# Kernel tuning notes

Measured on AMD Instinct MI355X. Metric: run time of the kernel, lower is better.

## Reference

```python
import jax, jax.numpy as jnp
import numpy as np

B, T, I, H, O = 128, 512, 64, 1024, 12

def setup_inputs() -> dict:
    key = jax.random.key(0)
    ks = jax.random.split(key, 7)
    s_ih = 1.0 / np.sqrt(H)
    return {
        "x": jax.random.normal(ks[0], (B, T, I), dtype=jnp.float32),
        "W_ih": jax.random.normal(ks[1], (H, I), dtype=jnp.float32) * s_ih,
        "W_hh": jax.random.normal(ks[2], (H, H), dtype=jnp.float32) * s_ih,
        "b_ih": jax.random.normal(ks[3], (H,), dtype=jnp.float32) * s_ih,
        "b_hh": jax.random.normal(ks[4], (H,), dtype=jnp.float32) * s_ih,
        "W_out": jax.random.normal(ks[5], (O, H), dtype=jnp.float32) * s_ih,
        "b_out": jax.random.normal(ks[6], (O,), dtype=jnp.float32) * s_ih,
    }

def reference(x, W_ih, W_hh, b_ih, b_hh, W_out, b_out):
    # x: [B, T, I] (batch_first). Vanilla tanh RNN, h0 = 0.
    Bn, Tn, _ = x.shape
    Hn = W_hh.shape[0]
    # Precompute input projections for all timesteps (batched GEMM).
    xp = jnp.einsum('bti,hi->tbh', x, W_ih) + b_ih + b_hh  # [T, B, H]
    h0 = jnp.zeros((Bn, Hn), dtype=x.dtype)

    def step(h, xt):
        h_new = jnp.tanh(xt + h @ W_hh.T)
        return h_new, h_new

    _, hs = jax.lax.scan(step, h0, xp)  # hs: [T, B, H]
    hs = jnp.swapaxes(hs, 0, 1)         # [B, T, H]
    out = jnp.einsum('bth,oh->bto', hs, W_out) + b_out  # [B, T, O]
    return out.reshape(-1, 12)
```

## Files before the change

kernel.cpp:

```cpp
#include <hip/hip_runtime.h>
#include <hip/hip_bf16.h>

#define B_ 128
#define T_ 512
#define I_ 64
#define H_ 1024
#define O_ 12
#define XSTEP (I_ * B_)
#define RSLOT 16384
#define TIMEOUT 2000
#define OSTRIDE 193

typedef __attribute__((ext_vector_type(8))) short bf16x8;
typedef __attribute__((ext_vector_type(4))) float f32x4;

#define MFMA16 __builtin_amdgcn_mfma_f32_16x16x32_bf16

__device__ __forceinline__ float bf2f(unsigned short s) {
  unsigned u = ((unsigned)s) << 16; float f; __builtin_memcpy(&f, &u, 4); return f;
}
__device__ __forceinline__ unsigned short f2bf(float f) {
  unsigned u; __builtin_memcpy(&u, &f, 4);
  u += 0x7fffu + ((u >> 16) & 1u);
  return (unsigned short)(u >> 16);
}

__device__ __forceinline__ unsigned ldA32(const unsigned* p) {
  return __hip_atomic_load(p, __ATOMIC_RELAXED, __HIP_MEMORY_SCOPE_AGENT);
}
__device__ __forceinline__ void stA32(unsigned* p, unsigned v) {
  __hip_atomic_store(p, v, __ATOMIC_RELAXED, __HIP_MEMORY_SCOPE_AGENT);
}
__device__ __forceinline__ unsigned long long ldA64(const unsigned long long* p) {
  return __hip_atomic_load(p, __ATOMIC_RELAXED, __HIP_MEMORY_SCOPE_AGENT);
}

__device__ __forceinline__ void store32_sc0(unsigned* p, unsigned v) {
  asm volatile("global_store_dword %0, %1, off sc0" :: "v"(p), "v"(v) : "memory");
}
__device__ __forceinline__ unsigned poll_sc0(const unsigned* p) {
  unsigned v;
  asm volatile("global_load_dword %0, %1, off sc0\n\ts_waitcnt vmcnt(0)"
               : "=v"(v) : "v"(p) : "memory");
  return v;
}
__device__ __forceinline__ bf16x8 load16_sc0(const void* p) {
  bf16x8 v;
  asm volatile("global_load_dwordx4 %0, %1, off sc0" : "=v"(v) : "v"(p));
  return v;
}
__device__ __forceinline__ void waitv8(bf16x8& v0, bf16x8& v1, bf16x8& v2, bf16x8& v3,
                                       bf16x8& v4, bf16x8& v5, bf16x8& v6, bf16x8& v7) {
  asm volatile("s_waitcnt vmcnt(0)"
               : "+v"(v0), "+v"(v1), "+v"(v2), "+v"(v3),
                 "+v"(v4), "+v"(v5), "+v"(v6), "+v"(v7) :: "memory");
}

__global__ void prep_xp(const float* __restrict__ x,
                        unsigned short* __restrict__ xPhi) {
  const int t = blockIdx.x;
  for (int u = threadIdx.x; u < 1024; u += 256) {
    const int ib = u >> 7, b = u & 127;
    const float* src = x + ((size_t)b * T_ + t) * I_ + ib * 8;
    bf16x8 hi;
    #pragma unroll
    for (int j = 0; j < 8; ++j) hi[j] = (short)f2bf(src[j]);
    *(bf16x8*)(xPhi + ((size_t)t * 1024 + u) * 8) = hi;
  }
}

__global__ void prep_misc(const float* __restrict__ b_out, float* __restrict__ out,
                          unsigned* __restrict__ bar) {
  const int idx = blockIdx.x * 256 + threadIdx.x;
  if (idx < 1024) bar[idx] = 0u;
  float bo[12];
  #pragma unroll
  for (int o = 0; o < 12; ++o) bo[o] = b_out[o];
  for (int r = idx; r < B_ * T_; r += 16384) {
    #pragma unroll
    for (int o = 0; o < 12; ++o) out[(size_t)r * 12 + o] = bo[o];
  }
}

__global__ __launch_bounds__(256, 1) void rnn_mfma(
    const float* __restrict__ W_ih, const float* __restrict__ W_hh,
    const float* __restrict__ b_ih, const float* __restrict__ b_hh,
    const float* __restrict__ W_out, const unsigned short* __restrict__ xPhi,
    unsigned short* __restrict__ rF, unsigned short* __restrict__ rS,
    unsigned* __restrict__ bar, float* __restrict__ out)
{
  __shared__ float part[4][544];
  __shared__ float outS[16 * OSTRIDE];
  __shared__ float biasS[32];
  __shared__ unsigned modeS;
  const int tid = threadIdx.x, bid = blockIdx.x;
  const int wave = tid >> 6, lane = tid & 63, quad = lane >> 4, ln = lane & 15;
  const int g = bid & 7, rg = bid >> 3;
  const int r0 = rg * 32, b0 = g * 16;
  if (tid < 32) biasS[tid] = b_ih[r0 + tid] + b_hh[r0 + tid];
  if (tid == 0) modeS = 1u;

  float wo[12][2];
  {
    const int R = r0 + (tid >> 4) * 2;
    #pragma unroll
    for (int o = 0; o < 12; ++o) {
      wo[o][0] = W_out[(size_t)o * H_ + R];
      wo[o][1] = W_out[(size_t)o * H_ + R + 1];
    }
  }

  bf16x8 ahhi[2][8], ahlo[2][8];
  #pragma unroll
  for (int mt = 0; mt < 2; ++mt)
    #pragma unroll
    for (int kt = 0; kt < 8; ++kt) {
      const float* wp = W_hh + (size_t)(r0 + mt * 16 + ln) * H_
                        + wave * 256 + kt * 32 + quad * 8;
      #pragma unroll
      for (int j = 0; j < 8; ++j) {
        float v = wp[j];
        unsigned short h = f2bf(v);
        ahhi[mt][kt][j] = (short)h;
        ahlo[mt][kt][j] = (short)f2bf(v - bf2f(h));
      }
    }
  bf16x8 axhi[2], axlo[2];
  if (wave < 2)
    #pragma unroll
    for (int mt = 0; mt < 2; ++mt) {
      const float* wp = W_ih + (size_t)(r0 + mt * 16 + ln) * I_
                        + wave * 32 + quad * 8;
      #pragma unroll
      for (int j = 0; j < 8; ++j) {
        float v = wp[j];
        unsigned short h = f2bf(v);
        axhi[mt][j] = (short)h;
        axlo[mt][j] = (short)f2bf(v - bf2f(h));
      }
    }
  __syncthreads();
  unsigned mode = 1u;

  const int bcol = b0 + ln;
  unsigned short* rFg = rF + (size_t)g * 2 * RSLOT;
  unsigned short* rSg = rS + (size_t)g * 2 * RSLOT;

  f32x4 xacc0 = {0.f, 0.f, 0.f, 0.f}, xacc1 = {0.f, 0.f, 0.f, 0.f};
  auto computeX = [&](int t) {
    if (wave < 2) {
      const size_t xo = (((size_t)t * 8 + wave * 4 + quad) * B_ + bcol) * 8;
      bf16x8 bxh = *(const bf16x8*)(xPhi + xo);
      f32x4 t0 = {0.f, 0.f, 0.f, 0.f}, t1 = {0.f, 0.f, 0.f, 0.f};
      t0 = MFMA16(axhi[0], bxh, t0, 0, 0, 0);
      t0 = MFMA16(axlo[0], bxh, t0, 0, 0, 0);
      t1 = MFMA16(axhi[1], bxh, t1, 0, 0, 0);
      t1 = MFMA16(axlo[1], bxh, t1, 0, 0, 0);
      xacc0 = t0; xacc1 = t1;
    }
  };
  computeX(0);

  auto outReduce = [&](int t) {
    if (tid >= 64) {
      const int j = tid - 64;
      const int n2 = j / 12, o = j - n2 * 12;
      float acc = 0.f;
      #pragma unroll
      for (int rp2 = 0; rp2 < 16; ++rp2)
        acc += outS[rp2 * OSTRIDE + n2 * 12 + o];
      atomicAdd(&out[((size_t)(b0 + n2) * T_ + t) * 12 + o], acc);
    }
  };

  for (int t = 0; t < T_; ++t) {
    f32x4 accA0 = xacc0, accA1 = xacc1;
    f32x4 accB0 = {0.f, 0.f, 0.f, 0.f}, accB1 = {0.f, 0.f, 0.f, 0.f};

    if (t > 0) {
      const int soff = ((wave * 32 + quad) * 16 + ln) * 8;
      bf16x8 bh[8];
      if (mode) {
        const unsigned short* slot = rFg + ((t - 1) & 1) * RSLOT + soff;
        #pragma unroll
        for (int kt = 0; kt < 8; ++kt)
          bh[kt] = load16_sc0(slot + kt * 512);
        waitv8(bh[0], bh[1], bh[2], bh[3], bh[4], bh[5], bh[6], bh[7]);
      } else {
        const unsigned long long* slot =
            (const unsigned long long*)(rSg + ((t - 1) & 1) * RSLOT + soff);
        #pragma unroll
        for (int kt = 0; kt < 8; ++kt) {
          union { unsigned long long u[2]; bf16x8 v; } U;
          U.u[0] = ldA64(slot + kt * 128);
          U.u[1] = ldA64(slot + kt * 128 + 1);
          bh[kt] = U.v;
        }
      }
      #pragma unroll
      for (int kt = 0; kt < 8; ++kt) {
        accA0 = MFMA16(ahhi[0][kt], bh[kt], accA0, 0, 0, 0);
        accA1 = MFMA16(ahhi[1][kt], bh[kt], accA1, 0, 0, 0);
        accB0 = MFMA16(ahlo[0][kt], bh[kt], accB0, 0, 0, 0);
        accB1 = MFMA16(ahlo[1][kt], bh[kt], accB1, 0, 0, 0);
      }
    }

    #pragma unroll
    for (int r = 0; r < 4; ++r) {
      part[wave][r * 68 + lane]       = accA0[r] + accB0[r];
      part[wave][(4 + r) * 68 + lane] = accA1[r] + accB1[r];
    }
    __syncthreads();

    {
      const int n = tid & 15, rp = tid >> 4;
      const int m0 = rp * 2;
      float hv[2];
      unsigned short o2[2];
      #pragma unroll
      for (int rr = 0; rr < 2; ++rr) {
        const int m = m0 + rr;
        const int f = ((m >> 4) * 4 + (m & 3)) * 68 + ((m >> 2) & 3) * 16 + n;
        float s = part[0][f] + part[1][f] + part[2][f] + part[3][f] + biasS[m];
        hv[rr] = tanhf(s);
        o2[rr] = f2bf(hv[rr]);
      }
      const unsigned pk = (unsigned)o2[0] | ((unsigned)o2[1] << 16);
      const int R = r0 + m0;
      const int soff = ((R >> 3) * 16 + n) * 8 + (R & 7);
      store32_sc0((unsigned*)(rFg + (t & 1) * RSLOT + soff), pk);
      stA32      ((unsigned*)(rSg + (t & 1) * RSLOT + soff), pk);
      #pragma unroll
      for (int o = 0; o < 12; ++o)
        outS[rp * OSTRIDE + n * 12 + o] = wo[o][0] * hv[0] + wo[o][1] * hv[1];
    }

    if (t < T_ - 1) {
      computeX(t + 1);
      asm volatile("s_waitcnt vmcnt(0)" ::: "memory");
      __syncthreads();
      if (tid == 0) {
        store32_sc0(&bar[g * 32 + rg],      (unsigned)(t + 1));
        stA32      (&bar[256 + g * 32 + rg], (unsigned)(t + 1));
      }
      if (tid < 64) {
        int ok = 0;
        if (mode) {
          for (int it = 0; it < TIMEOUT && !ok; ++it) {
            unsigned v = (lane < 32) ? poll_sc0(&bar[g * 32 + lane]) : 0xffffffffu;
            ok = __all((int)(v >= (unsigned)(t + 1)));
          }
        }
        if (!ok) {
          if (tid == 0) modeS = 0u;
          for (;;) {
            unsigned v = (lane < 32) ? ldA32(&bar[256 + g * 32 + lane]) : 0xffffffffu;
            if (__all((int)(v >= (unsigned)(t + 1)))) break;
            __builtin_amdgcn_s_sleep(1);
          }
        }
      } else {
        outReduce(t);
      }
      __syncthreads();
      mode = modeS;
    }
  }

  __syncthreads();
  outReduce(T_ - 1);
}

extern "C" void kernel_launch(void* const* d_in, const int* in_sizes, int n_in,
                              void* d_out, int out_size, void* d_ws, size_t ws_size,
                              hipStream_t stream)
{
  const float* x     = (const float*)d_in[0];
  const float* W_ih  = (const float*)d_in[1];
  const float* W_hh  = (const float*)d_in[2];
  const float* b_ih  = (const float*)d_in[3];
  const float* b_hh  = (const float*)d_in[4];
  const float* W_out = (const float*)d_in[5];
  const float* b_out = (const float*)d_in[6];
  float* out = (float*)d_out;

  unsigned short* xPhi = (unsigned short*)d_ws;
  unsigned short* rF   = xPhi + (size_t)T_ * XSTEP;
  unsigned short* rS   = rF + (size_t)8 * 2 * RSLOT;
  unsigned*       bar  = (unsigned*)(rS + (size_t)8 * 2 * RSLOT);

  prep_xp  <<<T_,  256, 0, stream>>>(x, xPhi);
  prep_misc<<<64,  256, 0, stream>>>(b_out, out, bar);
  rnn_mfma <<<256, 256, 0, stream>>>(W_ih, W_hh, b_ih, b_hh, W_out,
                                     xPhi, rF, rS, bar, out);
}
```

Baseline: 1.798 ms.

## Replace block-wide grid barrier with per-wave polling of producer flags

Each wave now waits only on the eight row-group flags whose hidden-state slices it actually reads, instead of wave 0 polling all 32 flags followed by a block-wide __syncthreads. The trailing __syncthreads after the barrier is removed, and the output reduction for the previous step is moved after the MFMA block and spread across all four waves. This is meant to shorten the critical path of each recurrent step by dropping a block sync and letting waves proceed independently. The fallback mode becomes per-wave rather than shared, and the outS read in the reduction now relies on the barrier before the next write to stay race-free.

```diff
diff --git a/kernel.cpp b/kernel.cpp
--- a/kernel.cpp
+++ b/kernel.cpp
@@ -92,13 +92,12 @@
   __shared__ float part[4][544];
   __shared__ float outS[16 * OSTRIDE];
   __shared__ float biasS[32];
-  __shared__ unsigned modeS;
   const int tid = threadIdx.x, bid = blockIdx.x;
   const int wave = tid >> 6, lane = tid & 63, quad = lane >> 4, ln = lane & 15;
   const int g = bid & 7, rg = bid >> 3;
   const int r0 = rg * 32, b0 = g * 16;
+  const int w8 = wave * 8;
   if (tid < 32) biasS[tid] = b_ih[r0 + tid] + b_hh[r0 + tid];
-  if (tid == 0) modeS = 1u;
 
   float wo[12][2];
   {
@@ -161,14 +160,14 @@
   };
   computeX(0);
 
-  auto outReduce = [&](int t) {
-    if (tid >= 64) {
-      const int j = tid - 64;
+  auto outReducePW = [&](int t) {
+    if (lane < 48) {
+      const int j = wave * 48 + lane;
       const int n2 = j / 12, o = j - n2 * 12;
       float acc = 0.f;
       #pragma unroll
       for (int rp2 = 0; rp2 < 16; ++rp2)
-        acc += outS[rp2 * OSTRIDE + n2 * 12 + o];
+        acc += outS[rp2 * OSTRIDE + j];
       atomicAdd(&out[((size_t)(b0 + n2) * T_ + t) * 12 + o], acc);
     }
   };
@@ -178,6 +177,24 @@
     f32x4 accB0 = {0.f, 0.f, 0.f, 0.f}, accB1 = {0.f, 0.f, 0.f, 0.f};
 
     if (t > 0) {
+      if (mode) {
+        int ok = 0;
+        for (int it = 0; it < TIMEOUT && !ok; ++it) {
+          unsigned v = (lane < 8) ? poll_sc0(&bar[g * 32 + w8 + lane])
+                                  : 0xffffffffu;
+          ok = __all((int)(v >= (unsigned)t));
+        }
+        if (!ok) mode = 0u;
+      }
+      if (!mode) {
+        for (;;) {
+          unsigned v = (lane < 8) ? ldA32(&bar[256 + g * 32 + w8 + lane])
+                                  : 0xffffffffu;
+          if (__all((int)(v >= (unsigned)t))) break;
+          __builtin_amdgcn_s_sleep(1);
+        }
+      }
+
       const int soff = ((wave * 32 + quad) * 16 + ln) * 8;
       bf16x8 bh[8];
       if (mode) {
@@ -204,6 +221,7 @@
         accB0 = MFMA16(ahlo[0][kt], bh[kt], accB0, 0, 0, 0);
         accB1 = MFMA16(ahlo[1][kt], bh[kt], accB1, 0, 0, 0);
       }
+      outReducePW(t - 1);
     }
 
     #pragma unroll
@@ -228,9 +246,9 @@
       }
       const unsigned pk = (unsigned)o2[0] | ((unsigned)o2[1] << 16);
       const int R = r0 + m0;
-      const int soff = ((R >> 3) * 16 + n) * 8 + (R & 7);
-      store32_sc0((unsigned*)(rFg + (t & 1) * RSLOT + soff), pk);
-      stA32      ((unsigned*)(rSg + (t & 1) * RSLOT + soff), pk);
+      const int soff2 = ((R >> 3) * 16 + n) * 8 + (R & 7);
+      store32_sc0((unsigned*)(rFg + (t & 1) * RSLOT + soff2), pk);
+      stA32      ((unsigned*)(rSg + (t & 1) * RSLOT + soff2), pk);
       #pragma unroll
       for (int o = 0; o < 12; ++o)
         outS[rp * OSTRIDE + n * 12 + o] = wo[o][0] * hv[0] + wo[o][1] * hv[1];
@@ -244,32 +262,11 @@
         store32_sc0(&bar[g * 32 + rg],      (unsigned)(t + 1));
         stA32      (&bar[256 + g * 32 + rg], (unsigned)(t + 1));
       }
-      if (tid < 64) {
-        int ok = 0;
-        if (mode) {
-          for (int it = 0; it < TIMEOUT && !ok; ++it) {
-            unsigned v = (lane < 32) ? poll_sc0(&bar[g * 32 + lane]) : 0xffffffffu;
-            ok = __all((int)(v >= (unsigned)(t + 1)));
-          }
-        }
-        if (!ok) {
-          if (tid == 0) modeS = 0u;
-          for (;;) {
-            unsigned v = (lane < 32) ? ldA32(&bar[256 + g * 32 + lane]) : 0xffffffffu;
-            if (__all((int)(v >= (unsigned)(t + 1)))) break;
-            __builtin_amdgcn_s_sleep(1);
-          }
-        }
-      } else {
-        outReduce(t);
-      }
-      __syncthreads();
-      mode = modeS;
     }
   }
 
   __syncthreads();
-  outReduce(T_ - 1);
+  outReducePW(T_ - 1);
 }
 
 extern "C" void kernel_launch(void* const* d_in, const int* in_sizes, int n_in,
```

After: 2.518 ms. 1.4x slower.
